# Kernel tuning notes

Hardware: AMD Instinct MI355X
Metric: run time of the kernel (lower is better)

Reference implementation:

```python
import jax, jax.numpy as jnp
import numpy as np

HEADS, KD = 8, 64
BN_EPS = 1e-3  # keras BatchNormalization default epsilon


def lstm(x, Wi, Wh, b, reverse=False):
    """Keras-style LSTM (gate order i,f,g,o). x: [B,S,D] -> ([B,S,H], [B,H])."""
    if reverse:
        x = x[:, ::-1, :]
    B = x.shape[0]
    H = Wh.shape[0]
    xw = jnp.einsum('bsd,dk->bsk', x, Wi) + b  # [B,S,4H]

    def step(carry, xt):
        h, c = carry
        z = xt + h @ Wh
        i, f, g, o = jnp.split(z, 4, axis=-1)
        c = jax.nn.sigmoid(f) * c + jax.nn.sigmoid(i) * jnp.tanh(g)
        h = jax.nn.sigmoid(o) * jnp.tanh(c)
        return (h, c), h

    init = (jnp.zeros((B, H), x.dtype), jnp.zeros((B, H), x.dtype))
    (hT, _), hs = jax.lax.scan(step, init, jnp.swapaxes(xw, 0, 1))
    hs = jnp.swapaxes(hs, 0, 1)
    if reverse:
        hs = hs[:, ::-1, :]  # align to forward time order (keras Bidirectional)
    return hs, hT


def mem_read(q, K, V):
    """Content-based read: softmax(qK^T/sqrt(d)) V. q:[B,64], K,V:[M,64]."""
    s = (q @ K.T) / jnp.sqrt(jnp.asarray(q.shape[-1], q.dtype))
    return jax.nn.softmax(s, axis=-1) @ V


def forward(tokens, emb, l1f_Wi, l1f_Wh, l1f_b, l1b_Wi, l1b_Wh, l1b_b,
            l2f_Wi, l2f_Wh, l2f_b, l2b_Wi, l2b_Wh, l2b_b,
            Wq, bq, Wk, bk, Wv, bv, Wo, bo, mq_W, mq_b,
            extK, extV, formK, formV, concK, concV, stmK, stmV,
            ltmK, ltmV, infK, infV, rs_W, rs_b, bn_g, bn_b, bn_m, bn_v,
            st_W, st_b, fo_W, fo_b):
    B = tokens.shape[0]
    x = emb[tokens]  # [B,S,64]
    # biLSTM 1 (return_sequences)
    f1, _ = lstm(x, l1f_Wi, l1f_Wh, l1f_b)
    b1, _ = lstm(x, l1b_Wi, l1b_Wh, l1b_b, reverse=True)
    x = jnp.concatenate([f1, b1], axis=-1)  # [B,S,1024]
    # biLSTM 2 (final state only)
    _, hf = lstm(x, l2f_Wi, l2f_Wh, l2f_b)
    _, hb = lstm(x, l2b_Wi, l2b_Wh, l2b_b, reverse=True)
    x = jnp.concatenate([hf, hb], axis=-1)  # [B,1024]
    # self-attention on length-1 sequence (expand_dims/squeeze in original)
    xq = x[:, None, :]
    q = (xq @ Wq + bq).reshape(B, 1, HEADS, KD)
    k = (xq @ Wk + bk).reshape(B, 1, HEADS, KD)
    v = (xq @ Wv + bv).reshape(B, 1, HEADS, KD)
    scores = jnp.einsum('bqhd,bkhd->bhqk', q, k) / jnp.sqrt(jnp.asarray(KD, x.dtype))
    attn = jax.nn.softmax(scores, axis=-1)
    ctx = jnp.einsum('bhqk,bkhd->bqhd', attn, v).reshape(B, 1, HEADS * KD)
    x = (ctx @ Wo + bo)[:, 0]  # [B,1024]
    # memory query + stage-dependent term extraction (stage = elementary1 -> idx 0..5)
    query = x @ mq_W + mq_b  # [B,64]
    terms = query[:, 0:6].sum(axis=-1)  # gather + reduce_sum
    reads = jnp.stack([
        mem_read(query, extK, extV),
        mem_read(query, formK, formV) * jax.nn.sigmoid(terms)[:, None],
        mem_read(query, concK, concV),
        mem_read(query, stmK, stmV),
        mem_read(query, ltmK, ltmV),
        mem_read(query, infK, infV),
    ], axis=1)  # [B,6,64]
    x = reads.mean(axis=1)  # [B,64]
    # reasoning + batchnorm (inference mode: running stats)
    x = jax.nn.relu(x @ rs_W + rs_b)
    x = bn_g * (x - bn_m) * jax.lax.rsqrt(bn_v + BN_EPS) + bn_b
    # stage output head + final sigmoid
    x = x @ st_W + st_b
    return jax.nn.sigmoid(x @ fo_W + fo_b)  # [B,1]


def setup_inputs():
    key = jax.random.key(0)
    ks = iter(jax.random.split(key, 64))
    rn = lambda shape, s=0.05: jax.random.normal(next(ks), shape, jnp.float32) * s
    inp = {}
    inp['tokens'] = jax.random.randint(next(ks), (512, 64), 0, 1000, jnp.int32)
    inp['emb'] = rn((1000, 64), 1.0)
    for p in ['l1f', 'l1b']:
        inp[p + '_Wi'] = rn((64, 2048)); inp[p + '_Wh'] = rn((512, 2048)); inp[p + '_b'] = jnp.zeros((2048,), jnp.float32)
    for p in ['l2f', 'l2b']:
        inp[p + '_Wi'] = rn((1024, 2048)); inp[p + '_Wh'] = rn((512, 2048)); inp[p + '_b'] = jnp.zeros((2048,), jnp.float32)
    for w, b in [('Wq', 'bq'), ('Wk', 'bk'), ('Wv', 'bv')]:
        inp[w] = rn((1024, 512)); inp[b] = jnp.zeros((512,), jnp.float32)
    inp['Wo'] = rn((512, 1024)); inp['bo'] = jnp.zeros((1024,), jnp.float32)
    inp['mq_W'] = rn((1024, 64)); inp['mq_b'] = jnp.zeros((64,), jnp.float32)
    for name, M in [('ext', 100), ('form', 1000), ('conc', 500), ('stm', 100), ('ltm', 10000), ('inf', 500)]:
        inp[name + 'K'] = rn((M, 64), 1.0); inp[name + 'V'] = rn((M, 64), 1.0)
    inp['rs_W'] = rn((64, 512)); inp['rs_b'] = jnp.zeros((512,), jnp.float32)
    inp['bn_g'] = jnp.ones((512,), jnp.float32); inp['bn_b'] = jnp.zeros((512,), jnp.float32)
    inp['bn_m'] = jnp.zeros((512,), jnp.float32); inp['bn_v'] = jnp.ones((512,), jnp.float32)
    inp['st_W'] = rn((512, 128)); inp['st_b'] = jnp.zeros((128,), jnp.float32)
    inp['fo_W'] = rn((128, 1)); inp['fo_b'] = jnp.zeros((1,), jnp.float32)
    return inp


def reference(tokens, emb, l1f_Wi, l1f_Wh, l1f_b, l1b_Wi, l1b_Wh, l1b_b,
              l2f_Wi, l2f_Wh, l2f_b, l2b_Wi, l2b_Wh, l2b_b,
              Wq, bq, Wk, bk, Wv, bv, Wo, bo, mq_W, mq_b,
              extK, extV, formK, formV, concK, concV, stmK, stmV,
              ltmK, ltmV, infK, infV, rs_W, rs_b, bn_g, bn_b, bn_m, bn_v,
              st_W, st_b, fo_W, fo_b):
    return forward(tokens, emb, l1f_Wi, l1f_Wh, l1f_b, l1b_Wi, l1b_Wh, l1b_b,
                   l2f_Wi, l2f_Wh, l2f_b, l2b_Wi, l2b_Wh, l2b_b,
                   Wq, bq, Wk, bk, Wv, bv, Wo, bo, mq_W, mq_b,
                   extK, extV, formK, formV, concK, concV, stmK, stmV,
                   ltmK, ltmV, infK, infV, rs_W, rs_b, bn_g, bn_b, bn_m, bn_v,
                   st_W, st_b, fo_W, fo_b)
```

## Files before the change

### kernel.cpp

```cpp
#include <hip/hip_runtime.h>
#include <math.h>

#define DEV __device__ __forceinline__

typedef __attribute__((ext_vector_type(8))) short short8v;
typedef __attribute__((ext_vector_type(4))) float f32x4;

DEV float sigf(float x){ return 1.0f/(1.0f+__expf(-x)); }

DEV void split_bf16(float v, short& hi, short& lo){
  union { float f; unsigned u; } a; a.f = v;
  unsigned rh = (a.u + 0x7FFFu + ((a.u >> 16) & 1u)) >> 16;
  hi = (short)rh;
  union { unsigned u; float f; } b; b.u = rh << 16;
  a.f = v - b.f;
  unsigned rl = (a.u + 0x7FFFu + ((a.u >> 16) & 1u)) >> 16;
  lo = (short)rl;
}

__global__ __launch_bounds__(256) void k_embed(const int* __restrict__ tok,
    const float* __restrict__ emb, float* __restrict__ x){
  int i = blockIdx.x*256 + threadIdx.x;
  int bs = i >> 6, d = i & 63;
  x[i] = emb[(size_t)tok[bs]*64 + d];
}

__global__ __launch_bounds__(256) void k_tsplit(const float* __restrict__ W,
    short* __restrict__ wth, short* __restrict__ wtl, int Ktot, int kbase){
  __shared__ float tile[32][33];
  int k0 = blockIdx.x*32, n0 = blockIdx.y*32;
  int tx = threadIdx.x & 31, ty = threadIdx.x >> 5;
  for (int r = ty; r < 32; r += 8)
    tile[r][tx] = W[(size_t)(k0+r)*2048 + n0 + tx];
  __syncthreads();
  for (int r = ty; r < 32; r += 8){
    int n = n0 + r;
    short hi, lo; split_bf16(tile[tx][r], hi, lo);
    size_t idx = (size_t)n*Ktot + kbase + k0 + tx;
    wth[idx] = hi; wtl[idx] = lo;
  }
}

struct StageArgs {
  const float *A0, *A1, *A2;
  int s0, s1, s2;
  int k1, k2;
  const short *wth, *wtl;
  int Ktot;
  const float* bias;
  float* c; float* hout; float* out1;
};

struct SMemStage {
  union {
    struct {
      short Ah[64][40];
      short Al[64][40];
      short Bh[128][40];
      short Bl[128][40];
    } st;
    float z[64][128];
  };
};

template<int NSEG>
DEV const float* a_ptr(const StageArgs& A, int k, int rowoff){
  if (NSEG == 2){
    if (k < A.k1) return A.A0 + (size_t)rowoff*A.s0 + k;
    return A.A1 + (size_t)rowoff*A.s1 + (k - A.k1);
  } else {
    if (k < A.k1) return A.A0 + (size_t)rowoff*A.s0 + k;
    if (k < A.k2) return A.A1 + (size_t)rowoff*A.s1 + (k - A.k1);
    return A.A2 + (size_t)rowoff*A.s2 + (k - A.k2);
  }
}

template<int NSEG>
__global__ __launch_bounds__(256) void k_lstm_mfma(StageArgs fa, StageArgs ba){
  StageArgs A = blockIdx.z ? ba : fa;
  __shared__ SMemStage s;
  const int tid = threadIdx.x;
  const int lane = tid & 63, w = tid >> 6;
  const int wr = w >> 1, wc = w & 1;
  const int m0 = blockIdx.y * 64, j0 = blockIdx.x * 32;
  const int sArow = tid >> 2, sAoff = (tid & 3) * 8;
  const int sBrow = tid >> 1, sBpart = tid & 1;
  const int nB = (sBrow & 3) * 512 + j0 + (sBrow >> 2);
  const short* wtB = (sBpart ? A.wtl : A.wth) + (size_t)nB * A.Ktot;
  const int fAr = wr*32 + (lane & 15), fk = (lane >> 4) * 8;
  const int fBc = wc*64 + (lane & 15);

  f32x4 acc[2][4];
  #pragma unroll
  for (int i=0;i<2;++i)
    #pragma unroll
    for (int j=0;j<4;++j) acc[i][j] = 0.f;

  float4 av0, av1; short8v bv[4];
  {
    const float* ap = a_ptr<NSEG>(A, 0, m0 + sArow) + sAoff;
    av0 = *(const float4*)ap; av1 = *(const float4*)(ap+4);
    #pragma unroll
    for (int i=0;i<4;++i) bv[i] = *(const short8v*)(wtB + i*8);
  }

  for (int k0 = 0; k0 < A.Ktot; k0 += 32){
    __syncthreads();
    {
      float a8[8] = {av0.x,av0.y,av0.z,av0.w,av1.x,av1.y,av1.z,av1.w};
      short8v h8, l8;
      #pragma unroll
      for (int i=0;i<8;++i){ short hh, ll; split_bf16(a8[i], hh, ll); h8[i]=hh; l8[i]=ll; }
      *(short8v*)&s.st.Ah[sArow][sAoff] = h8;
      *(short8v*)&s.st.Al[sArow][sAoff] = l8;
      short (*Bp)[40] = sBpart ? s.st.Bl : s.st.Bh;
      #pragma unroll
      for (int i=0;i<4;++i) *(short8v*)&Bp[sBrow][i*8] = bv[i];
    }
    __syncthreads();
    int kn = k0 + 32;
    if (kn < A.Ktot){
      const float* ap = a_ptr<NSEG>(A, kn, m0 + sArow) + sAoff;
      av0 = *(const float4*)ap; av1 = *(const float4*)(ap+4);
      #pragma unroll
      for (int i=0;i<4;++i) bv[i] = *(const short8v*)(wtB + kn + i*8);
    }
    short8v ah[2], al[2], bh[4], bl[4];
    #pragma unroll
    for (int mf=0;mf<2;++mf){
      ah[mf] = *(const short8v*)&s.st.Ah[fAr + mf*16][fk];
      al[mf] = *(const short8v*)&s.st.Al[fAr + mf*16][fk];
    }
    #pragma unroll
    for (int nf=0;nf<4;++nf){
      bh[nf] = *(const short8v*)&s.st.Bh[fBc + nf*16][fk];
      bl[nf] = *(const short8v*)&s.st.Bl[fBc + nf*16][fk];
    }
    #pragma unroll
    for (int mf=0;mf<2;++mf)
      #pragma unroll
      for (int nf=0;nf<4;++nf){
        acc[mf][nf] = __builtin_amdgcn_mfma_f32_16x16x32_bf16(ah[mf], bh[nf], acc[mf][nf], 0,0,0);
        acc[mf][nf] = __builtin_amdgcn_mfma_f32_16x16x32_bf16(ah[mf], bl[nf], acc[mf][nf], 0,0,0);
        acc[mf][nf] = __builtin_amdgcn_mfma_f32_16x16x32_bf16(al[mf], bh[nf], acc[mf][nf], 0,0,0);
      }
  }

  __syncthreads();
  #pragma unroll
  for (int mf=0;mf<2;++mf)
    #pragma unroll
    for (int nf=0;nf<4;++nf)
      #pragma unroll
      for (int r=0;r<4;++r)
        s.z[wr*32 + mf*16 + (lane>>4)*4 + r][wc*64 + nf*16 + (lane&15)] = acc[mf][nf][r];
  __syncthreads();

  {
    int row = tid >> 2, jjq = (tid & 3) * 8;
    size_t rbase = (size_t)(m0+row)*512 + j0;
    #pragma unroll
    for (int q=0;q<2;++q){
      int jj4 = jjq + q*4;
      float4 cold = *(const float4*)(A.c + rbase + jj4);
      float co[4] = {cold.x, cold.y, cold.z, cold.w};
      float hn[4], cn[4];
      #pragma unroll
      for (int e=0;e<4;++e){
        int jj = jj4 + e, n = j0 + jj;
        float4 zv = *(const float4*)&s.z[row][jj*4];
        float zi = zv.x + A.bias[n];
        float zf = zv.y + A.bias[512+n];
        float zg = zv.z + A.bias[1024+n];
        float zo = zv.w + A.bias[1536+n];
        float cc = sigf(zf)*co[e] + sigf(zi)*tanhf(zg);
        cn[e] = cc; hn[e] = sigf(zo)*tanhf(cc);
      }
      *(float4*)(A.c    + rbase + jj4) = make_float4(cn[0],cn[1],cn[2],cn[3]);
      *(float4*)(A.hout + rbase + jj4) = make_float4(hn[0],hn[1],hn[2],hn[3]);
      if (A.out1)
        *(float4*)(A.out1 + (size_t)(m0+row)*32768 + j0 + jj4) = make_float4(hn[0],hn[1],hn[2],hn[3]);
    }
  }
}

template<int ACT>
__global__ __launch_bounds__(256) void k_gemm(const float* __restrict__ A,
    const float* __restrict__ W, const float* __restrict__ bias,
    float* __restrict__ C, int K, int N){
  __shared__ float As[16][68];
  __shared__ float Ws[16][68];
  int tid=threadIdx.x;
  int m0=blockIdx.y*64, n0=blockIdx.x*64;
  int ar=tid>>2, akq=(tid&3)*4;
  int wk=tid>>4, wcq=(tid&15)*4;
  int ty=tid>>4, tx=tid&15;
  float acc[4][4];
  #pragma unroll
  for(int r=0;r<4;++r){ 
    #pragma unroll
    for(int c=0;c<4;++c) acc[r][c]=0.f; }
  for(int k0=0;k0<K;k0+=16){
    float4 av=*(const float4*)(A+(size_t)(m0+ar)*K+(k0+akq));
    float4 wv=*(const float4*)(W+(size_t)(k0+wk)*N+(n0+wcq));
    __syncthreads();
    As[akq+0][ar]=av.x; As[akq+1][ar]=av.y; As[akq+2][ar]=av.z; As[akq+3][ar]=av.w;
    *(float4*)&Ws[wk][wcq]=wv;
    __syncthreads();
    #pragma unroll
    for(int kk=0;kk<16;++kk){
      float4 a4=*(const float4*)&As[kk][ty*4];
      float4 b4=*(const float4*)&Ws[kk][tx*4];
      float a[4]={a4.x,a4.y,a4.z,a4.w};
      float b[4]={b4.x,b4.y,b4.z,b4.w};
      #pragma unroll
      for(int r=0;r<4;++r){
        #pragma unroll
        for(int c=0;c<4;++c) acc[r][c]+=a[r]*b[c]; }
    }
  }
  #pragma unroll
  for(int r=0;r<4;++r){
    int row=m0+ty*4+r;
    float o[4];
    #pragma unroll
    for(int c=0;c<4;++c){
      float v=acc[r][c]+bias[n0+tx*4+c];
      if(ACT==1) v=fmaxf(v,0.f);
      o[c]=v;
    }
    *(float4*)(C+(size_t)row*N+n0+tx*4) = make_float4(o[0],o[1],o[2],o[3]);
  }
}

__global__ __launch_bounds__(256) void k_concat(const float* __restrict__ hf,
    const float* __restrict__ hb, float* __restrict__ x2){
  int i = blockIdx.x*256+threadIdx.x;
  int b = i>>10, j=i&1023;
  x2[i] = (j<512) ? hf[b*512+j] : hb[b*512 + (j-512)];
}

__global__ __launch_bounds__(256) void k_mem_part(const float* __restrict__ query,
    const float* K0,const float* V0,const float* K1,const float* V1,
    const float* K2,const float* V2,const float* K3,const float* V3,
    const float* K4,const float* V4,const float* K5,const float* V5,
    float* __restrict__ parts){
  int chunk = blockIdx.x, b0 = blockIdx.y*8, tid = threadIdx.x;
  const float *Kp, *Vp; int mstart, mcnt;
  if      (chunk==0){ Kp=K0; Vp=V0; mstart=0;              mcnt=100; }
  else if (chunk<5) { Kp=K1; Vp=V1; mstart=(chunk-1)*250;  mcnt=250; }
  else if (chunk<7) { Kp=K2; Vp=V2; mstart=(chunk-5)*250;  mcnt=250; }
  else if (chunk==7){ Kp=K3; Vp=V3; mstart=0;              mcnt=100; }
  else if (chunk<48){ Kp=K4; Vp=V4; mstart=(chunk-8)*250;  mcnt=250; }
  else              { Kp=K5; Vp=V5; mstart=(chunk-48)*250; mcnt=250; }
  __shared__ float qs[8][64];
  __shared__ float p[8][256];
  __shared__ float red[4][8][64];
  __shared__ float mv[8], sv[8];
  ((float*)qs)[tid]     = query[(size_t)b0*64 + tid];
  ((float*)qs)[tid+256] = query[(size_t)b0*64 + 256 + tid];
  __syncthreads();
  float dot[8] = {0,0,0,0,0,0,0,0};
  if (tid < mcnt){
    const float4* kr = (const float4*)(Kp + (size_t)(mstart+tid)*64);
    #pragma unroll 4
    for (int i=0;i<16;++i){
      float4 kv = kr[i];
      #pragma unroll
      for (int mb=0;mb<8;++mb){
        float4 qv = *(const float4*)&qs[mb][i*4];
        dot[mb] += kv.x*qv.x + kv.y*qv.y + kv.z*qv.z + kv.w*qv.w;
      }
    }
  }
  #pragma unroll
  for (int mb=0;mb<8;++mb) p[mb][tid] = dot[mb]*0.125f;
  __syncthreads();
  {
    int mb = tid >> 5, l32 = tid & 31;
    float mx = -1e30f;
    #pragma unroll
    for (int j=0;j<8;++j){ int m = l32 + j*32; if (m < mcnt) mx = fmaxf(mx, p[mb][m]); }
    for (int d=16; d; d>>=1) mx = fmaxf(mx, __shfl_xor(mx, d, 32));
    float sum = 0.f;
    #pragma unroll
    for (int j=0;j<8;++j){ int m = l32 + j*32;
      if (m < mcnt){ float e = __expf(p[mb][m]-mx); p[mb][m]=e; sum+=e; } }
    for (int d=16; d; d>>=1) sum += __shfl_xor(sum, d, 32);
    if (l32==0){ mv[mb]=mx; sv[mb]=sum; }
  }
  __syncthreads();
  int d = tid & 63, g = tid >> 6;
  float pv[8] = {0,0,0,0,0,0,0,0};
  for (int m=g; m<mcnt; m+=4){
    float vv = Vp[(size_t)(mstart+m)*64 + d];
    #pragma unroll
    for (int mb=0;mb<8;++mb) pv[mb] += p[mb][m]*vv;
  }
  #pragma unroll
  for (int mb=0;mb<8;++mb) red[g][mb][d] = pv[mb];
  __syncthreads();
  for (int i=tid; i<512; i+=256){
    int mb = i >> 6, dd = i & 63;
    float tot = red[0][mb][dd]+red[1][mb][dd]+red[2][mb][dd]+red[3][mb][dd];
    parts[((size_t)(b0+mb)*50 + chunk)*68 + dd] = tot;
  }
  if (tid < 8){
    parts[((size_t)(b0+tid)*50 + chunk)*68 + 64] = mv[tid];
    parts[((size_t)(b0+tid)*50 + chunk)*68 + 65] = sv[tid];
  }
}

__global__ __launch_bounds__(64) void k_mem_comb(const float* __restrict__ query,
    const float* __restrict__ parts, float* __restrict__ reads){
  int b = blockIdx.x, d = threadIdx.x;
  const int c0s[6] = {0,1,5,7,8,48};
  const int c1s[6] = {1,5,7,8,48,50};
  float t = 0.f;
  #pragma unroll
  for (int i=0;i<6;++i) t += query[(size_t)b*64+i];
  float wt1 = sigf(t);
  for (int mem=0; mem<6; ++mem){
    float gmax = -1e30f;
    for (int c=c0s[mem]; c<c1s[mem]; ++c)
      gmax = fmaxf(gmax, parts[((size_t)b*50+c)*68 + 64]);
    float pv=0.f, tot=0.f;
    for (int c=c0s[mem]; c<c1s[mem]; ++c){
      const float* pc = parts + ((size_t)b*50+c)*68;
      float sc = __expf(pc[64]-gmax);
      pv  += sc*pc[d];
      tot += sc*pc[65];
    }
    float r = pv/tot * (mem==1 ? wt1 : 1.0f);
    reads[((size_t)mem*512+b)*64 + d] = r;
  }
}

__global__ __launch_bounds__(256) void k_meanreads(const float* __restrict__ reads,
    float* __restrict__ rmean){
  int i = blockIdx.x*256+threadIdx.x;
  float sm=0.f;
  #pragma unroll
  for(int mem=0;mem<6;++mem) sm+=reads[(size_t)mem*32768 + i];
  rmean[i]=sm*(1.0f/6.0f);
}

__global__ __launch_bounds__(256) void k_bn(const float* __restrict__ x,
    const float* __restrict__ g,const float* __restrict__ b,
    const float* __restrict__ m,const float* __restrict__ v,
    float* __restrict__ y){
  int i=blockIdx.x*256+threadIdx.x;
  int j=i&511;
  y[i] = g[j]*(x[i]-m[j])*rsqrtf(v[j]+1e-3f)+b[j];
}

__global__ __launch_bounds__(256) void k_final(const float* __restrict__ x6,
    const float* __restrict__ foW, const float* __restrict__ fob,
    float* __restrict__ out){
  int b = blockIdx.x*256+threadIdx.x;
  float acc=fob[0];
  #pragma unroll 4
  for(int k=0;k<128;++k) acc += x6[(size_t)b*128+k]*foW[k];
  out[b] = 1.0f/(1.0f+__expf(-acc));
}

extern "C" void kernel_launch(void* const* d_in, const int* in_sizes, int n_in,
                              void* d_out, int out_size, void* d_ws, size_t ws_size,
                              hipStream_t stream){
  const int*   tokens = (const int*)  d_in[0];
  const float* emb    = (const float*)d_in[1];
  const float* l1f_Wi=(const float*)d_in[2], *l1f_Wh=(const float*)d_in[3], *l1f_b=(const float*)d_in[4];
  const float* l1b_Wi=(const float*)d_in[5], *l1b_Wh=(const float*)d_in[6], *l1b_b=(const float*)d_in[7];
  const float* l2f_Wi=(const float*)d_in[8], *l2f_Wh=(const float*)d_in[9], *l2f_b=(const float*)d_in[10];
  const float* l2b_Wi=(const float*)d_in[11],*l2b_Wh=(const float*)d_in[12],*l2b_b=(const float*)d_in[13];
  const float* Wv =(const float*)d_in[18], *bv =(const float*)d_in[19];
  const float* Wo =(const float*)d_in[20], *bo =(const float*)d_in[21];
  const float* mqW=(const float*)d_in[22], *mqb=(const float*)d_in[23];
  const float* extK =(const float*)d_in[24], *extV =(const float*)d_in[25];
  const float* formK=(const float*)d_in[26], *formV=(const float*)d_in[27];
  const float* concK=(const float*)d_in[28], *concV=(const float*)d_in[29];
  const float* stmK =(const float*)d_in[30], *stmV =(const float*)d_in[31];
  const float* ltmK =(const float*)d_in[32], *ltmV =(const float*)d_in[33];
  const float* infK =(const float*)d_in[34], *infV =(const float*)d_in[35];
  const float* rsW=(const float*)d_in[36], *rsb=(const float*)d_in[37];
  const float* bng=(const float*)d_in[38], *bnb=(const float*)d_in[39];
  const float* bnm=(const float*)d_in[40], *bnv=(const float*)d_in[41];
  const float* stW=(const float*)d_in[42], *stb=(const float*)d_in[43];
  const float* foW=(const float*)d_in[44], *fob=(const float*)d_in[45];
  float* out = (float*)d_out;

  float* ws = (float*)d_ws;
  const size_t S = 262144;
  float* hf[2]  = {ws+0*S, ws+1*S};
  float* hb[2]  = {ws+2*S, ws+3*S};
  float* cf = ws+4*S;  float* cb = ws+5*S;
  float* h2f[2] = {ws+6*S, ws+7*S};
  float* h2b[2] = {ws+8*S, ws+9*S};
  float* c2f = ws+10*S; float* c2b = ws+11*S;
  float* x     = ws+12*S;
  float* f1    = ws+20*S;
  float* b1    = ws+84*S;
  float* x2    = ws+148*S;
  float* vbuf  = ws+150*S;
  float* x3    = ws+151*S;
  float* query = ws+153*S;
  float* reads = query+32768;
  float* rmean = reads+196608;
  float* x4    = rmean+32768;
  float* x5    = x4+S;
  float* x6    = x5+S;
  float* parts = x6+65536;
  short* wt    = (short*)(parts + (size_t)512*50*68);
  short* l1fH = wt;                 short* l1fL = l1fH + (size_t)2048*576;
  short* l1bH = l1fL + (size_t)2048*576;  short* l1bL = l1bH + (size_t)2048*576;
  short* l2fH = l1bL + (size_t)2048*576;  short* l2fL = l2fH + (size_t)2048*1536;
  short* l2bH = l2fL + (size_t)2048*1536; short* l2bL = l2bH + (size_t)2048*1536;

  hipMemsetAsync(ws, 0, 12*S*sizeof(float), stream);

  k_tsplit<<<dim3(2,64),  256, 0, stream>>>(l1f_Wi, l1fH, l1fL, 576, 0);
  k_tsplit<<<dim3(16,64), 256, 0, stream>>>(l1f_Wh, l1fH, l1fL, 576, 64);
  k_tsplit<<<dim3(2,64),  256, 0, stream>>>(l1b_Wi, l1bH, l1bL, 576, 0);
  k_tsplit<<<dim3(16,64), 256, 0, stream>>>(l1b_Wh, l1bH, l1bL, 576, 64);
  k_tsplit<<<dim3(32,64), 256, 0, stream>>>(l2f_Wi, l2fH, l2fL, 1536, 0);
  k_tsplit<<<dim3(16,64), 256, 0, stream>>>(l2f_Wh, l2fH, l2fL, 1536, 1024);
  k_tsplit<<<dim3(32,64), 256, 0, stream>>>(l2b_Wi, l2bH, l2bL, 1536, 0);
  k_tsplit<<<dim3(16,64), 256, 0, stream>>>(l2b_Wh, l2bH, l2bL, 1536, 1024);

  k_embed<<<2097152/256, 256, 0, stream>>>(tokens, emb, x);

  for (int t=0; t<64; ++t){
    int sr = 63-t;
    StageArgs fa{}, ba{};
    fa.A0 = x + (size_t)t*64;  fa.s0 = 4096;
    fa.A1 = hf[t&1];           fa.s1 = 512;
    fa.k1 = 64; fa.k2 = 0;
    fa.wth = l1fH; fa.wtl = l1fL; fa.Ktot = 576; fa.bias = l1f_b;
    fa.c = cf; fa.hout = hf[(t+1)&1]; fa.out1 = f1 + (size_t)t*512;
    ba.A0 = x + (size_t)sr*64; ba.s0 = 4096;
    ba.A1 = hb[t&1];           ba.s1 = 512;
    ba.k1 = 64; ba.k2 = 0;
    ba.wth = l1bH; ba.wtl = l1bL; ba.Ktot = 576; ba.bias = l1b_b;
    ba.c = cb; ba.hout = hb[(t+1)&1]; ba.out1 = b1 + (size_t)sr*512;
    k_lstm_mfma<2><<<dim3(16,8,2), 256, 0, stream>>>(fa, ba);
  }
  for (int t=0; t<64; ++t){
    int sr = 63-t;
    StageArgs fa{}, ba{};
    fa.A0 = f1 + (size_t)t*512; fa.s0 = 32768;
    fa.A1 = b1 + (size_t)t*512; fa.s1 = 32768;
    fa.A2 = h2f[t&1];           fa.s2 = 512;
    fa.k1 = 512; fa.k2 = 1024;
    fa.wth = l2fH; fa.wtl = l2fL; fa.Ktot = 1536; fa.bias = l2f_b;
    fa.c = c2f; fa.hout = h2f[(t+1)&1]; fa.out1 = nullptr;
    ba.A0 = f1 + (size_t)sr*512; ba.s0 = 32768;
    ba.A1 = b1 + (size_t)sr*512; ba.s1 = 32768;
    ba.A2 = h2b[t&1];            ba.s2 = 512;
    ba.k1 = 512; ba.k2 = 1024;
    ba.wth = l2bH; ba.wtl = l2bL; ba.Ktot = 1536; ba.bias = l2b_b;
    ba.c = c2b; ba.hout = h2b[(t+1)&1]; ba.out1 = nullptr;
    k_lstm_mfma<3><<<dim3(16,8,2), 256, 0, stream>>>(fa, ba);
  }

  k_concat<<<524288/256, 256, 0, stream>>>(h2f[0], h2b[0], x2);
  k_gemm<0><<<dim3(8,8),  256, 0, stream>>>(x2,    Wv,  bv,  vbuf,  1024, 512);
  k_gemm<0><<<dim3(16,8), 256, 0, stream>>>(vbuf,  Wo,  bo,  x3,    512,  1024);
  k_gemm<0><<<dim3(1,8),  256, 0, stream>>>(x3,    mqW, mqb, query, 1024, 64);
  k_mem_part<<<dim3(50,64), 256, 0, stream>>>(query, extK,extV, formK,formV, concK,concV,
                                              stmK,stmV, ltmK,ltmV, infK,infV, parts);
  k_mem_comb<<<512, 64, 0, stream>>>(query, parts, reads);
  k_meanreads<<<32768/256, 256, 0, stream>>>(reads, rmean);
  k_gemm<1><<<dim3(8,8),  256, 0, stream>>>(rmean, rsW, rsb, x4,    64,   512);
  k_bn<<<262144/256, 256, 0, stream>>>(x4, bng, bnb, bnm, bnv, x5);
  k_gemm<0><<<dim3(2,8),  256, 0, stream>>>(x5,    stW, stb, x6,    512,  128);
  k_final<<<2, 256, 0, stream>>>(x6, foW, fob, out);
}
```

Before: 6.541 ms.

## Fuse LSTM timestep launches into one cooperative persistent kernel with bf16 activations

Replaces the 128 per-timestep kernel launches for both biLSTM layers with a single cooperative kernel that loops over time and uses grid-wide syncs between steps. Activations (embeddings and hidden states) are now stored pre-split into bf16 hi/lo pairs, so the GEMM A-operand loads no longer re-split fp32 values every k-tile and move half as many bytes. The layer-1 outputs are written only as hi/lo shorts and read back directly by layer 2. It adds a dependency on grid.sync cost and on all 256 blocks being co-resident.

```diff
diff --git a/kernel.cpp b/kernel.cpp
--- a/kernel.cpp
+++ b/kernel.cpp
@@ -1,5 +1,8 @@
 #include <hip/hip_runtime.h>
+#include <hip/hip_cooperative_groups.h>
 #include <math.h>
+
+namespace cg = cooperative_groups;
 
 #define DEV __device__ __forceinline__
 
@@ -18,11 +21,13 @@
   lo = (short)rl;
 }
 
-__global__ __launch_bounds__(256) void k_embed(const int* __restrict__ tok,
-    const float* __restrict__ emb, float* __restrict__ x){
+__global__ __launch_bounds__(256) void k_embed_split(const int* __restrict__ tok,
+    const float* __restrict__ emb, short* __restrict__ xH, short* __restrict__ xL){
   int i = blockIdx.x*256 + threadIdx.x;
   int bs = i >> 6, d = i & 63;
-  x[i] = emb[(size_t)tok[bs]*64 + d];
+  float v = emb[(size_t)tok[bs]*64 + d];
+  short h,l; split_bf16(v,h,l);
+  xH[i]=h; xL[i]=l;
 }
 
 __global__ __launch_bounds__(256) void k_tsplit(const float* __restrict__ W,
@@ -40,16 +45,6 @@
     wth[idx] = hi; wtl[idx] = lo;
   }
 }
-
-struct StageArgs {
-  const float *A0, *A1, *A2;
-  int s0, s1, s2;
-  int k1, k2;
-  const short *wth, *wtl;
-  int Ktot;
-  const float* bias;
-  float* c; float* hout; float* out1;
-};
 
 struct SMemStage {
   union {
@@ -63,124 +58,180 @@
   };
 };
 
-template<int NSEG>
-DEV const float* a_ptr(const StageArgs& A, int k, int rowoff){
-  if (NSEG == 2){
-    if (k < A.k1) return A.A0 + (size_t)rowoff*A.s0 + k;
-    return A.A1 + (size_t)rowoff*A.s1 + (k - A.k1);
-  } else {
-    if (k < A.k1) return A.A0 + (size_t)rowoff*A.s0 + k;
-    if (k < A.k2) return A.A1 + (size_t)rowoff*A.s1 + (k - A.k1);
-    return A.A2 + (size_t)rowoff*A.s2 + (k - A.k2);
-  }
-}
-
-template<int NSEG>
-__global__ __launch_bounds__(256) void k_lstm_mfma(StageArgs fa, StageArgs ba){
-  StageArgs A = blockIdx.z ? ba : fa;
+struct RecStep {
+  const short *a0H,*a0L,*a1H,*a1L,*a2H,*a2L;
+  int s0,s1,s2;
+  const short *wH,*wL;
+  const float *bias;
+  float *cst;
+  short *oH,*oL;
+  float *ofp;
+};
+
+template<int KTOT>
+DEV void rec_step(const RecStep& P, SMemStage& s, int m0, int j0, int tid){
+  const int lane=tid&63, w=tid>>6, wr=w>>1, wc=w&1;
+  const int cB=tid>>1, pB=tid&1;
+  const int nB=(cB&3)*512 + j0 + (cB>>2);
+  const short* wtB = (pB? P.wL : P.wH) + (size_t)nB*KTOT;
+  const int rA=tid&63, pA=(tid>>6)&1;
+  const bool doA = tid<128;
+  const int arow = m0 + rA;
+  const int fAr = wr*32 + (lane&15), fk=(lane>>4)*8;
+  const int fBc = wc*64 + (lane&15);
+
+  f32x4 acc[2][4];
+  #pragma unroll
+  for(int i=0;i<2;++i){
+    #pragma unroll
+    for(int j=0;j<4;++j) acc[i][j]=0.f;
+  }
+
+  auto abase=[&](int k0)->const short*{
+    if (KTOT==576){
+      if (k0<64) return (pA? P.a0L:P.a0H) + (size_t)arow*P.s0 + k0;
+      return (pA? P.a1L:P.a1H) + (size_t)arow*P.s1 + (k0-64);
+    } else {
+      if (k0<512)  return (pA? P.a0L:P.a0H) + (size_t)arow*P.s0 + k0;
+      if (k0<1024) return (pA? P.a1L:P.a1H) + (size_t)arow*P.s1 + (k0-512);
+      return (pA? P.a2L:P.a2H) + (size_t)arow*P.s2 + (k0-1024);
+    }
+  };
+
+  short8v bvv[4], avv[4];
+  #pragma unroll
+  for(int i=0;i<4;++i) bvv[i]=*(const short8v*)(wtB+i*8);
+  if (doA){ const short* ap=abase(0);
+    #pragma unroll
+    for(int i=0;i<4;++i) avv[i]=*(const short8v*)(ap+i*8); }
+
+  for (int k0=0;k0<KTOT;k0+=32){
+    __syncthreads();
+    { short (*Bp)[40] = pB ? s.st.Bl : s.st.Bh;
+      #pragma unroll
+      for(int i=0;i<4;++i) *(short8v*)&Bp[cB][i*8]=bvv[i];
+      if (doA){ short (*Ap)[40] = pA ? s.st.Al : s.st.Ah;
+        #pragma unroll
+        for(int i=0;i<4;++i) *(short8v*)&Ap[rA][i*8]=avv[i]; } }
+    __syncthreads();
+    int kn=k0+32;
+    if (kn<KTOT){
+      #pragma unroll
+      for(int i=0;i<4;++i) bvv[i]=*(const short8v*)(wtB+kn+i*8);
+      if (doA){ const short* ap=abase(kn);
+        #pragma unroll
+        for(int i=0;i<4;++i) avv[i]=*(const short8v*)(ap+i*8); } }
+    short8v ah[2],al[2],bh[4],bl[4];
+    #pragma unroll
+    for(int mf=0;mf<2;++mf){
+      ah[mf]=*(const short8v*)&s.st.Ah[fAr+mf*16][fk];
+      al[mf]=*(const short8v*)&s.st.Al[fAr+mf*16][fk]; }
+    #pragma unroll
+    for(int nf=0;nf<4;++nf){
+      bh[nf]=*(const short8v*)&s.st.Bh[fBc+nf*16][fk];
+      bl[nf]=*(const short8v*)&s.st.Bl[fBc+nf*16][fk]; }
+    #pragma unroll
+    for(int mf=0;mf<2;++mf){
+      #pragma unroll
+      for(int nf=0;nf<4;++nf){
+        acc[mf][nf]=__builtin_amdgcn_mfma_f32_16x16x32_bf16(ah[mf],bh[nf],acc[mf][nf],0,0,0);
+        acc[mf][nf]=__builtin_amdgcn_mfma_f32_16x16x32_bf16(ah[mf],bl[nf],acc[mf][nf],0,0,0);
+        acc[mf][nf]=__builtin_amdgcn_mfma_f32_16x16x32_bf16(al[mf],bh[nf],acc[mf][nf],0,0,0);
+      }
+    }
+  }
+
+  __syncthreads();
+  #pragma unroll
+  for(int mf=0;mf<2;++mf){
+    #pragma unroll
+    for(int nf=0;nf<4;++nf){
+      #pragma unroll
+      for(int r=0;r<4;++r)
+        s.z[wr*32+mf*16+(lane>>4)*4+r][wc*64+nf*16+(lane&15)] = acc[mf][nf][r];
+    }
+  }
+  __syncthreads();
+  {
+    int row=tid>>2, jq=(tid&3)*8;
+    size_t rbase=(size_t)(m0+row)*512 + j0;
+    #pragma unroll
+    for(int q=0;q<2;++q){
+      int jj4=jq+q*4;
+      float4 cold=*(const float4*)(P.cst+rbase+jj4);
+      float co[4]={cold.x,cold.y,cold.z,cold.w};
+      float hn[4],cn[4];
+      #pragma unroll
+      for(int e=0;e<4;++e){
+        int jj=jj4+e, n=j0+jj;
+        float4 zv=*(const float4*)&s.z[row][jj*4];
+        float zi=zv.x+P.bias[n];
+        float zf=zv.y+P.bias[512+n];
+        float zg=zv.z+P.bias[1024+n];
+        float zo=zv.w+P.bias[1536+n];
+        float cc=sigf(zf)*co[e]+sigf(zi)*tanhf(zg);
+        cn[e]=cc; hn[e]=sigf(zo)*tanhf(cc);
+      }
+      *(float4*)(P.cst+rbase+jj4)=make_float4(cn[0],cn[1],cn[2],cn[3]);
+      short hh[4],hl[4];
+      #pragma unroll
+      for(int e=0;e<4;++e) split_bf16(hn[e],hh[e],hl[e]);
+      *(short4*)(P.oH+rbase+jj4)=make_short4(hh[0],hh[1],hh[2],hh[3]);
+      *(short4*)(P.oL+rbase+jj4)=make_short4(hl[0],hl[1],hl[2],hl[3]);
+      if (P.ofp) *(float4*)(P.ofp+rbase+jj4)=make_float4(hn[0],hn[1],hn[2],hn[3]);
+    }
+  }
+}
+
+struct RecArgs {
+  const short *xH,*xL;
+  const short *w1H[2],*w1L[2];
+  const short *w2H[2],*w2L[2];
+  const float *b1v[2],*b2v[2];
+  short *f1H,*f1L,*g1H,*g1L;
+  const short *zeroS;
+  short *h2H[2][2],*h2L[2][2];
+  float *c1[2],*c2[2];
+  float *h2out[2];
+};
+
+__global__ __launch_bounds__(256) void k_recur(RecArgs A){
+  cg::grid_group grid = cg::this_grid();
   __shared__ SMemStage s;
-  const int tid = threadIdx.x;
-  const int lane = tid & 63, w = tid >> 6;
-  const int wr = w >> 1, wc = w & 1;
-  const int m0 = blockIdx.y * 64, j0 = blockIdx.x * 32;
-  const int sArow = tid >> 2, sAoff = (tid & 3) * 8;
-  const int sBrow = tid >> 1, sBpart = tid & 1;
-  const int nB = (sBrow & 3) * 512 + j0 + (sBrow >> 2);
-  const short* wtB = (sBpart ? A.wtl : A.wth) + (size_t)nB * A.Ktot;
-  const int fAr = wr*32 + (lane & 15), fk = (lane >> 4) * 8;
-  const int fBc = wc*64 + (lane & 15);
-
-  f32x4 acc[2][4];
-  #pragma unroll
-  for (int i=0;i<2;++i)
-    #pragma unroll
-    for (int j=0;j<4;++j) acc[i][j] = 0.f;
-
-  float4 av0, av1; short8v bv[4];
-  {
-    const float* ap = a_ptr<NSEG>(A, 0, m0 + sArow) + sAoff;
-    av0 = *(const float4*)ap; av1 = *(const float4*)(ap+4);
-    #pragma unroll
-    for (int i=0;i<4;++i) bv[i] = *(const short8v*)(wtB + i*8);
-  }
-
-  for (int k0 = 0; k0 < A.Ktot; k0 += 32){
-    __syncthreads();
-    {
-      float a8[8] = {av0.x,av0.y,av0.z,av0.w,av1.x,av1.y,av1.z,av1.w};
-      short8v h8, l8;
-      #pragma unroll
-      for (int i=0;i<8;++i){ short hh, ll; split_bf16(a8[i], hh, ll); h8[i]=hh; l8[i]=ll; }
-      *(short8v*)&s.st.Ah[sArow][sAoff] = h8;
-      *(short8v*)&s.st.Al[sArow][sAoff] = l8;
-      short (*Bp)[40] = sBpart ? s.st.Bl : s.st.Bh;
-      #pragma unroll
-      for (int i=0;i<4;++i) *(short8v*)&Bp[sBrow][i*8] = bv[i];
-    }
-    __syncthreads();
-    int kn = k0 + 32;
-    if (kn < A.Ktot){
-      const float* ap = a_ptr<NSEG>(A, kn, m0 + sArow) + sAoff;
-      av0 = *(const float4*)ap; av1 = *(const float4*)(ap+4);
-      #pragma unroll
-      for (int i=0;i<4;++i) bv[i] = *(const short8v*)(wtB + kn + i*8);
-    }
-    short8v ah[2], al[2], bh[4], bl[4];
-    #pragma unroll
-    for (int mf=0;mf<2;++mf){
-      ah[mf] = *(const short8v*)&s.st.Ah[fAr + mf*16][fk];
-      al[mf] = *(const short8v*)&s.st.Al[fAr + mf*16][fk];
-    }
-    #pragma unroll
-    for (int nf=0;nf<4;++nf){
-      bh[nf] = *(const short8v*)&s.st.Bh[fBc + nf*16][fk];
-      bl[nf] = *(const short8v*)&s.st.Bl[fBc + nf*16][fk];
-    }
-    #pragma unroll
-    for (int mf=0;mf<2;++mf)
-      #pragma unroll
-      for (int nf=0;nf<4;++nf){
-        acc[mf][nf] = __builtin_amdgcn_mfma_f32_16x16x32_bf16(ah[mf], bh[nf], acc[mf][nf], 0,0,0);
-        acc[mf][nf] = __builtin_amdgcn_mfma_f32_16x16x32_bf16(ah[mf], bl[nf], acc[mf][nf], 0,0,0);
-        acc[mf][nf] = __builtin_amdgcn_mfma_f32_16x16x32_bf16(al[mf], bh[nf], acc[mf][nf], 0,0,0);
-      }
-  }
-
-  __syncthreads();
-  #pragma unroll
-  for (int mf=0;mf<2;++mf)
-    #pragma unroll
-    for (int nf=0;nf<4;++nf)
-      #pragma unroll
-      for (int r=0;r<4;++r)
-        s.z[wr*32 + mf*16 + (lane>>4)*4 + r][wc*64 + nf*16 + (lane&15)] = acc[mf][nf][r];
-  __syncthreads();
-
-  {
-    int row = tid >> 2, jjq = (tid & 3) * 8;
-    size_t rbase = (size_t)(m0+row)*512 + j0;
-    #pragma unroll
-    for (int q=0;q<2;++q){
-      int jj4 = jjq + q*4;
-      float4 cold = *(const float4*)(A.c + rbase + jj4);
-      float co[4] = {cold.x, cold.y, cold.z, cold.w};
-      float hn[4], cn[4];
-      #pragma unroll
-      for (int e=0;e<4;++e){
-        int jj = jj4 + e, n = j0 + jj;
-        float4 zv = *(const float4*)&s.z[row][jj*4];
-        float zi = zv.x + A.bias[n];
-        float zf = zv.y + A.bias[512+n];
-        float zg = zv.z + A.bias[1024+n];
-        float zo = zv.w + A.bias[1536+n];
-        float cc = sigf(zf)*co[e] + sigf(zi)*tanhf(zg);
-        cn[e] = cc; hn[e] = sigf(zo)*tanhf(cc);
-      }
-      *(float4*)(A.c    + rbase + jj4) = make_float4(cn[0],cn[1],cn[2],cn[3]);
-      *(float4*)(A.hout + rbase + jj4) = make_float4(hn[0],hn[1],hn[2],hn[3]);
-      if (A.out1)
-        *(float4*)(A.out1 + (size_t)(m0+row)*32768 + j0 + jj4) = make_float4(hn[0],hn[1],hn[2],hn[3]);
-    }
+  const int tid=threadIdx.x;
+  const int j0=blockIdx.x*32, m0=blockIdx.y*64, dir=blockIdx.z;
+  const size_t SL=262144;
+  short* outH = dir? A.g1H : A.f1H;
+  short* outL = dir? A.g1L : A.f1L;
+  for (int t=0;t<64;++t){
+    int sidx = dir? 63-t : t;
+    RecStep P;
+    P.a0H=A.xH + sidx*64; P.a0L=A.xL + sidx*64; P.s0=4096;
+    if (t==0){ P.a1H=A.zeroS; P.a1L=A.zeroS; }
+    else { int sp = dir? sidx+1 : sidx-1;
+           P.a1H=outH + (size_t)sp*SL; P.a1L=outL + (size_t)sp*SL; }
+    P.s1=512;
+    P.a2H=nullptr; P.a2L=nullptr; P.s2=0;
+    P.wH=A.w1H[dir]; P.wL=A.w1L[dir]; P.bias=A.b1v[dir];
+    P.cst=A.c1[dir];
+    P.oH=outH+(size_t)sidx*SL; P.oL=outL+(size_t)sidx*SL; P.ofp=nullptr;
+    rec_step<576>(P,s,m0,j0,tid);
+    grid.sync();
+  }
+  for (int t=0;t<64;++t){
+    int sidx = dir? 63-t : t;
+    RecStep P;
+    P.a0H=A.f1H+(size_t)sidx*SL; P.a0L=A.f1L+(size_t)sidx*SL; P.s0=512;
+    P.a1H=A.g1H+(size_t)sidx*SL; P.a1L=A.g1L+(size_t)sidx*SL; P.s1=512;
+    int pp=t&1;
+    if (t==0){ P.a2H=A.zeroS; P.a2L=A.zeroS; }
+    else { P.a2H=A.h2H[dir][pp^1]; P.a2L=A.h2L[dir][pp^1]; }
+    P.s2=512;
+    P.wH=A.w2H[dir]; P.wL=A.w2L[dir]; P.bias=A.b2v[dir];
+    P.cst=A.c2[dir];
+    P.oH=A.h2H[dir][pp]; P.oL=A.h2L[dir][pp]; P.ofp=A.h2out[dir];
+    rec_step<1536>(P,s,m0,j0,tid);
+    grid.sync();
   }
 }
 
@@ -197,7 +248,7 @@
   int ty=tid>>4, tx=tid&15;
   float acc[4][4];
   #pragma unroll
-  for(int r=0;r<4;++r){ 
+  for(int r=0;r<4;++r){
     #pragma unroll
     for(int c=0;c<4;++c) acc[r][c]=0.f; }
   for(int k0=0;k0<K;k0+=16){
@@ -389,80 +440,68 @@
   const float* foW=(const float*)d_in[44], *fob=(const float*)d_in[45];
   float* out = (float*)d_out;
 
-  float* ws = (float*)d_ws;
-  const size_t S = 262144;
-  float* hf[2]  = {ws+0*S, ws+1*S};
-  float* hb[2]  = {ws+2*S, ws+3*S};
-  float* cf = ws+4*S;  float* cb = ws+5*S;
-  float* h2f[2] = {ws+6*S, ws+7*S};
-  float* h2b[2] = {ws+8*S, ws+9*S};
-  float* c2f = ws+10*S; float* c2b = ws+11*S;
-  float* x     = ws+12*S;
-  float* f1    = ws+20*S;
-  float* b1    = ws+84*S;
-  float* x2    = ws+148*S;
-  float* vbuf  = ws+150*S;
-  float* x3    = ws+151*S;
-  float* query = ws+153*S;
-  float* reads = query+32768;
-  float* rmean = reads+196608;
-  float* x4    = rmean+32768;
-  float* x5    = x4+S;
-  float* x6    = x5+S;
-  float* parts = x6+65536;
-  short* wt    = (short*)(parts + (size_t)512*50*68);
-  short* l1fH = wt;                 short* l1fL = l1fH + (size_t)2048*576;
-  short* l1bH = l1fL + (size_t)2048*576;  short* l1bL = l1bH + (size_t)2048*576;
-  short* l2fH = l1bL + (size_t)2048*576;  short* l2fL = l2fH + (size_t)2048*1536;
-  short* l2bH = l2fL + (size_t)2048*1536; short* l2bL = l2bH + (size_t)2048*1536;
-
-  hipMemsetAsync(ws, 0, 12*S*sizeof(float), stream);
-
-  k_tsplit<<<dim3(2,64),  256, 0, stream>>>(l1f_Wi, l1fH, l1fL, 576, 0);
-  k_tsplit<<<dim3(16,64), 256, 0, stream>>>(l1f_Wh, l1fH, l1fL, 576, 64);
-  k_tsplit<<<dim3(2,64),  256, 0, stream>>>(l1b_Wi, l1bH, l1bL, 576, 0);
-  k_tsplit<<<dim3(16,64), 256, 0, stream>>>(l1b_Wh, l1bH, l1bL, 576, 64);
-  k_tsplit<<<dim3(32,64), 256, 0, stream>>>(l2f_Wi, l2fH, l2fL, 1536, 0);
-  k_tsplit<<<dim3(16,64), 256, 0, stream>>>(l2f_Wh, l2fH, l2fL, 1536, 1024);
-  k_tsplit<<<dim3(32,64), 256, 0, stream>>>(l2b_Wi, l2bH, l2bL, 1536, 0);
-  k_tsplit<<<dim3(16,64), 256, 0, stream>>>(l2b_Wh, l2bH, l2bL, 1536, 1024);
-
-  k_embed<<<2097152/256, 256, 0, stream>>>(tokens, emb, x);
-
-  for (int t=0; t<64; ++t){
-    int sr = 63-t;
-    StageArgs fa{}, ba{};
-    fa.A0 = x + (size_t)t*64;  fa.s0 = 4096;
-    fa.A1 = hf[t&1];           fa.s1 = 512;
-    fa.k1 = 64; fa.k2 = 0;
-    fa.wth = l1fH; fa.wtl = l1fL; fa.Ktot = 576; fa.bias = l1f_b;
-    fa.c = cf; fa.hout = hf[(t+1)&1]; fa.out1 = f1 + (size_t)t*512;
-    ba.A0 = x + (size_t)sr*64; ba.s0 = 4096;
-    ba.A1 = hb[t&1];           ba.s1 = 512;
-    ba.k1 = 64; ba.k2 = 0;
-    ba.wth = l1bH; ba.wtl = l1bL; ba.Ktot = 576; ba.bias = l1b_b;
-    ba.c = cb; ba.hout = hb[(t+1)&1]; ba.out1 = b1 + (size_t)sr*512;
-    k_lstm_mfma<2><<<dim3(16,8,2), 256, 0, stream>>>(fa, ba);
-  }
-  for (int t=0; t<64; ++t){
-    int sr = 63-t;
-    StageArgs fa{}, ba{};
-    fa.A0 = f1 + (size_t)t*512; fa.s0 = 32768;
-    fa.A1 = b1 + (size_t)t*512; fa.s1 = 32768;
-    fa.A2 = h2f[t&1];           fa.s2 = 512;
-    fa.k1 = 512; fa.k2 = 1024;
-    fa.wth = l2fH; fa.wtl = l2fL; fa.Ktot = 1536; fa.bias = l2f_b;
-    fa.c = c2f; fa.hout = h2f[(t+1)&1]; fa.out1 = nullptr;
-    ba.A0 = f1 + (size_t)sr*512; ba.s0 = 32768;
-    ba.A1 = b1 + (size_t)sr*512; ba.s1 = 32768;
-    ba.A2 = h2b[t&1];            ba.s2 = 512;
-    ba.k1 = 512; ba.k2 = 1024;
-    ba.wth = l2bH; ba.wtl = l2bL; ba.Ktot = 1536; ba.bias = l2b_b;
-    ba.c = c2b; ba.hout = h2b[(t+1)&1]; ba.out1 = nullptr;
-    k_lstm_mfma<3><<<dim3(16,8,2), 256, 0, stream>>>(fa, ba);
-  }
-
-  k_concat<<<524288/256, 256, 0, stream>>>(h2f[0], h2b[0], x2);
+  char* p = (char*)d_ws;
+  auto alloc = [&](size_t bytes)->void*{ void* r=p; p += (bytes + 255) & ~(size_t)255; return r; };
+
+  short* zeroS = (short*)alloc(512*512*2);
+  float* c1f = (float*)alloc(1<<20);
+  float* c1b = (float*)alloc(1<<20);
+  float* c2f = (float*)alloc(1<<20);
+  float* c2b = (float*)alloc(1<<20);
+  short* xH  = (short*)alloc((size_t)2097152*2);
+  short* xL  = (short*)alloc((size_t)2097152*2);
+  short* f1H = (short*)alloc((size_t)64*512*512*2);
+  short* f1L = (short*)alloc((size_t)64*512*512*2);
+  short* g1H = (short*)alloc((size_t)64*512*512*2);
+  short* g1L = (short*)alloc((size_t)64*512*512*2);
+  short* h2Hb[2][2]; short* h2Lb[2][2];
+  for (int d=0; d<2; ++d)
+    for (int q=0; q<2; ++q){ h2Hb[d][q]=(short*)alloc(512*512*2); h2Lb[d][q]=(short*)alloc(512*512*2); }
+  float* h2o0 = (float*)alloc(1<<20);
+  float* h2o1 = (float*)alloc(1<<20);
+  short* w1H0=(short*)alloc((size_t)2048*576*2);  short* w1L0=(short*)alloc((size_t)2048*576*2);
+  short* w1H1=(short*)alloc((size_t)2048*576*2);  short* w1L1=(short*)alloc((size_t)2048*576*2);
+  short* w2H0=(short*)alloc((size_t)2048*1536*2); short* w2L0=(short*)alloc((size_t)2048*1536*2);
+  short* w2H1=(short*)alloc((size_t)2048*1536*2); short* w2L1=(short*)alloc((size_t)2048*1536*2);
+  float* x2    = (float*)alloc((size_t)512*1024*4);
+  float* vbuf  = (float*)alloc((size_t)512*512*4);
+  float* x3    = (float*)alloc((size_t)512*1024*4);
+  float* query = (float*)alloc((size_t)512*64*4);
+  float* reads = (float*)alloc((size_t)6*512*64*4);
+  float* rmean = (float*)alloc((size_t)512*64*4);
+  float* x4    = (float*)alloc((size_t)512*512*4);
+  float* x5    = (float*)alloc((size_t)512*512*4);
+  float* x6    = (float*)alloc((size_t)512*128*4);
+  float* parts = (float*)alloc((size_t)512*50*68*4);
+
+  hipMemsetAsync(zeroS, 0, 512*512*2 + 4*(1<<20), stream);
+
+  k_tsplit<<<dim3(2,64),  256, 0, stream>>>(l1f_Wi, w1H0, w1L0, 576, 0);
+  k_tsplit<<<dim3(16,64), 256, 0, stream>>>(l1f_Wh, w1H0, w1L0, 576, 64);
+  k_tsplit<<<dim3(2,64),  256, 0, stream>>>(l1b_Wi, w1H1, w1L1, 576, 0);
+  k_tsplit<<<dim3(16,64), 256, 0, stream>>>(l1b_Wh, w1H1, w1L1, 576, 64);
+  k_tsplit<<<dim3(32,64), 256, 0, stream>>>(l2f_Wi, w2H0, w2L0, 1536, 0);
+  k_tsplit<<<dim3(16,64), 256, 0, stream>>>(l2f_Wh, w2H0, w2L0, 1536, 1024);
+  k_tsplit<<<dim3(32,64), 256, 0, stream>>>(l2b_Wi, w2H1, w2L1, 1536, 0);
+  k_tsplit<<<dim3(16,64), 256, 0, stream>>>(l2b_Wh, w2H1, w2L1, 1536, 1024);
+
+  k_embed_split<<<2097152/256, 256, 0, stream>>>(tokens, emb, xH, xL);
+
+  RecArgs ra;
+  ra.xH=xH; ra.xL=xL;
+  ra.w1H[0]=w1H0; ra.w1L[0]=w1L0; ra.w1H[1]=w1H1; ra.w1L[1]=w1L1;
+  ra.w2H[0]=w2H0; ra.w2L[0]=w2L0; ra.w2H[1]=w2H1; ra.w2L[1]=w2L1;
+  ra.b1v[0]=l1f_b; ra.b1v[1]=l1b_b; ra.b2v[0]=l2f_b; ra.b2v[1]=l2b_b;
+  ra.f1H=f1H; ra.f1L=f1L; ra.g1H=g1H; ra.g1L=g1L;
+  ra.zeroS=zeroS;
+  for (int d=0; d<2; ++d)
+    for (int q=0; q<2; ++q){ ra.h2H[d][q]=h2Hb[d][q]; ra.h2L[d][q]=h2Lb[d][q]; }
+  ra.c1[0]=c1f; ra.c1[1]=c1b; ra.c2[0]=c2f; ra.c2[1]=c2b;
+  ra.h2out[0]=h2o0; ra.h2out[1]=h2o1;
+  void* kargs[] = { &ra };
+  hipLaunchCooperativeKernel((void*)k_recur, dim3(16,8,2), dim3(256,1,1), kargs, 0, stream);
+
+  k_concat<<<524288/256, 256, 0, stream>>>(h2o0, h2o1, x2);
   k_gemm<0><<<dim3(8,8),  256, 0, stream>>>(x2,    Wv,  bv,  vbuf,  1024, 512);
   k_gemm<0><<<dim3(16,8), 256, 0, stream>>>(vbuf,  Wo,  bo,  x3,    512,  1024);
   k_gemm<0><<<dim3(1,8),  256, 0, stream>>>(x3,    mqW, mqb, query, 1024, 64);
```

Result: slower. 10.38 ms (+58.7%).
